# Kernel tuning notes

Measured on AMD Instinct MI355X. Metric: run time of the kernel, lower is better.

The kernel has to match this reference:

```python
import jax, jax.numpy as jnp
import numpy as np
from jax import lax

B, C_IN, H, W = 32, 3, 224, 224
EMBED = 768 // 4  # dim // 4 = 192
K = 3             # kernel_size
STRIDE = 2        # patch_stride
PAD = 1           # patch_padding
BN_EPS = 1e-5


def setup_inputs() -> dict:
    key = jax.random.key(0)
    kx, kw, kb, kg, kbeta = jax.random.split(key, 5)
    x = jax.random.normal(kx, (B, C_IN, H, W), dtype=jnp.float32)
    fan_in = C_IN * K * K
    bound = 1.0 / np.sqrt(fan_in)
    conv_w = jax.random.uniform(kw, (EMBED, C_IN, K, K), jnp.float32, -bound, bound)
    conv_b = jax.random.uniform(kb, (EMBED,), jnp.float32, -bound, bound)
    gamma = jnp.ones((EMBED,), jnp.float32)
    beta = jnp.zeros((EMBED,), jnp.float32)
    return {"x": x, "conv_w": conv_w, "conv_b": conv_b, "gamma": gamma, "beta": beta}


def _patch_embed(x, conv_w, conv_b, gamma, beta):
    # Conv2d(in_chans, embed_dim, k=3, stride=2, pad=1)
    y = lax.conv_general_dilated(
        x, conv_w,
        window_strides=(STRIDE, STRIDE),
        padding=[(PAD, PAD), (PAD, PAD)],
        dimension_numbers=("NCHW", "OIHW", "NCHW"),
    ) + conv_b[None, :, None, None]  # [B, EMBED, 112, 112]
    # BatchNorm2d (training mode: batch statistics, biased variance)
    mean = jnp.mean(y, axis=(0, 2, 3), keepdims=True)
    var = jnp.mean(jnp.square(y - mean), axis=(0, 2, 3), keepdims=True)
    y = (y - mean) * lax.rsqrt(var + BN_EPS)
    y = y * gamma[None, :, None, None] + beta[None, :, None, None]
    # GELU (torch default: exact erf form)
    y = jax.nn.gelu(y, approximate=False)
    # MaxPool2d(kernel=3, stride=2, padding=1)
    y = lax.reduce_window(
        y, -jnp.inf, lax.max,
        window_dimensions=(1, 1, 3, 3),
        window_strides=(1, 1, STRIDE, STRIDE),
        padding=[(0, 0), (0, 0), (PAD, PAD), (PAD, PAD)],
    )  # [B, EMBED, 56, 56]
    return y


def reference(x, conv_w, conv_b, gamma, beta):
    return _patch_embed(x, conv_w, conv_b, gamma, beta)
```

## Files before the change

### kernel.cpp

```cpp
#include <hip/hip_runtime.h>
#include <hip/hip_bf16.h>
#include <math.h>

#define B_   32
#define CIN  3
#define H_   224
#define W_   224
#define OC   192
#define OH   112
#define OW   112
#define PH   56
#define PW   56
#define NSP  (B_*OH*OW)
#define PLANE (OH*OW)

static __device__ __forceinline__ unsigned short f2bf(float f) {
    __hip_bfloat16 h = __float2bfloat16(f);
    return *reinterpret_cast<unsigned short*>(&h);
}
static __device__ __forceinline__ float bfbits2f(unsigned short u) {
    unsigned int v = ((unsigned int)u) << 16;
    return *reinterpret_cast<float*>(&v);
}
static __device__ __forceinline__ float bf_lo(unsigned int u) {
    unsigned int v = u << 16;
    return *reinterpret_cast<float*>(&v);
}
static __device__ __forceinline__ float bf_hi(unsigned int u) {
    unsigned int v = u & 0xffff0000u;
    return *reinterpret_cast<float*>(&v);
}

static __device__ __forceinline__ float fexp2(float x) {
#if __has_builtin(__builtin_amdgcn_exp2f)
    return __builtin_amdgcn_exp2f(x);
#else
    return exp2f(x);
#endif
}
static __device__ __forceinline__ float frcp(float x) {
#if __has_builtin(__builtin_amdgcn_rcpf)
    return __builtin_amdgcn_rcpf(x);
#else
    return 1.0f / x;
#endif
}

static __device__ __forceinline__ float fast_gelu(float x) {
    float x2 = x * x;
    float inner = fmaf(0.044715f * x2, x, x);
    float e = fexp2(inner * 2.3022082f);
    float r = frcp(1.0f + e);
    return x * (e * r);
}

__global__ void zero_stats(float* stats) {
    for (int i = threadIdx.x; i < 384; i += 256) stats[i] = 0.f;
}

__global__ __launch_bounds__(256) void conv_kernel(
    const float* __restrict__ x, const float* __restrict__ w,
    const float* __restrict__ bias, __hip_bfloat16* __restrict__ y)
{
    int g = blockIdx.x * 256 + threadIdx.x;
    int ow = g % OW;
    int t  = g / OW;
    int oh = t % OH;
    int b  = t / OH;

    int ih0 = 2 * oh - 1;
    int iw0 = 2 * ow - 1;

    float xv[CIN][3][3];
    #pragma unroll
    for (int c = 0; c < CIN; ++c) {
        #pragma unroll
        for (int r = 0; r < 3; ++r) {
            int ih = ih0 + r;
            bool rv = (ih >= 0) && (ih < H_);
            const float* xrow = x + (((size_t)b * CIN + c) * H_ + (rv ? ih : 0)) * W_;
            #pragma unroll
            for (int j = 0; j < 3; ++j) {
                int iw = iw0 + j;
                bool v = rv && (iw >= 0) && (iw < W_);
                xv[c][r][j] = v ? xrow[iw] : 0.f;
            }
        }
    }

    unsigned short* yp = reinterpret_cast<unsigned short*>(y) +
                         (size_t)b * OC * PLANE + oh * OW + ow;

    #pragma unroll 2
    for (int oc = 0; oc < OC; ++oc) {
        float a = bias[oc];
        const float* wp = w + oc * 27;
        #pragma unroll
        for (int c = 0; c < CIN; ++c)
            #pragma unroll
            for (int r = 0; r < 3; ++r)
                #pragma unroll
                for (int j = 0; j < 3; ++j)
                    a = fmaf(wp[c * 9 + r * 3 + j], xv[c][r][j], a);
        yp[(size_t)oc * PLANE] = f2bf(a);
    }
}

__global__ __launch_bounds__(256) void stats_kernel(
    const __hip_bfloat16* __restrict__ y, float* __restrict__ stats)
{
    int plane = blockIdx.x;
    int oc = plane % OC;
    const unsigned int* p =
        reinterpret_cast<const unsigned int*>(y) + plane * (PLANE / 2);

    float s = 0.f, s2 = 0.f;
    for (int ch = threadIdx.x; ch < PLANE / 8; ch += 256) {
        uint4 v = reinterpret_cast<const uint4*>(p)[ch];
        unsigned int u[4] = {v.x, v.y, v.z, v.w};
        #pragma unroll
        for (int k = 0; k < 4; ++k) {
            float lo = bf_lo(u[k]);
            float hi = bf_hi(u[k]);
            s  += lo + hi;
            s2 += lo * lo + hi * hi;
        }
    }

    __shared__ float ls[256], ls2[256];
    int tid = threadIdx.x;
    ls[tid] = s; ls2[tid] = s2;
    __syncthreads();
    for (int off = 128; off > 0; off >>= 1) {
        if (tid < off) { ls[tid] += ls[tid + off]; ls2[tid] += ls2[tid + off]; }
        __syncthreads();
    }
    if (tid == 0) {
        atomicAdd(&stats[oc], ls[0]);
        atomicAdd(&stats[OC + oc], ls2[0]);
    }
}

__global__ __launch_bounds__(256) void pool_kernel(
    const __hip_bfloat16* __restrict__ y, const float* __restrict__ stats,
    const float* __restrict__ gamma, const float* __restrict__ beta,
    float* __restrict__ out)
{
    int g = blockIdx.x * 256 + threadIdx.x;
    int j  = g % (PW / 4);
    int t  = g / (PW / 4);
    int ph = t % PH;
    int plane = t / PH;
    int oc = plane % OC;

    const unsigned int* p32 =
        reinterpret_cast<const unsigned int*>(y) + (size_t)plane * (PLANE / 2);

    int bi  = 4 * j - 1;
    int bi0 = (bi < 0) ? 0 : bi;

    float cmax[10], cmin[10];
    #pragma unroll
    for (int c = 0; c < 10; ++c) { cmax[c] = -INFINITY; cmin[c] = INFINITY; }

    #pragma unroll
    for (int rr = 0; rr < 3; ++rr) {
        int ih = 2 * ph - 1 + rr;
        if (ih >= 0) {
            const unsigned int* rp = p32 + ih * (OW / 2);
            unsigned int u0 = rp[bi0];
            unsigned int u1 = rp[bi + 1];
            unsigned int u2 = rp[bi + 2];
            unsigned int u3 = rp[bi + 3];
            unsigned int u4 = rp[bi + 4];
            float f0 = bf_lo(u0), f1 = bf_hi(u0);
            float f2 = bf_lo(u1), f3 = bf_hi(u1);
            float f4 = bf_lo(u2), f5 = bf_hi(u2);
            float f6 = bf_lo(u3), f7 = bf_hi(u3);
            float f8 = bf_lo(u4), f9 = bf_hi(u4);
            cmax[0] = fmaxf(cmax[0], f0); cmin[0] = fminf(cmin[0], f0);
            cmax[1] = fmaxf(cmax[1], f1); cmin[1] = fminf(cmin[1], f1);
            cmax[2] = fmaxf(cmax[2], f2); cmin[2] = fminf(cmin[2], f2);
            cmax[3] = fmaxf(cmax[3], f3); cmin[3] = fminf(cmin[3], f3);
            cmax[4] = fmaxf(cmax[4], f4); cmin[4] = fminf(cmin[4], f4);
            cmax[5] = fmaxf(cmax[5], f5); cmin[5] = fminf(cmin[5], f5);
            cmax[6] = fmaxf(cmax[6], f6); cmin[6] = fminf(cmin[6], f6);
            cmax[7] = fmaxf(cmax[7], f7); cmin[7] = fminf(cmin[7], f7);
            cmax[8] = fmaxf(cmax[8], f8); cmin[8] = fminf(cmin[8], f8);
            cmax[9] = fmaxf(cmax[9], f9); cmin[9] = fminf(cmin[9], f9);
        }
    }
    if (j == 0) { cmax[1] = -INFINITY; cmin[1] = INFINITY; }

    float mean = stats[oc] * (1.0f / (float)NSP);
    float var  = fmaf(-mean, mean, stats[OC + oc] * (1.0f / (float)NSP));
    float inv  = rsqrtf(var + 1e-5f);
    float sc   = gamma[oc] * inv;
    float sh   = fmaf(-mean, sc, beta[oc]);

    float4 res;
    float* rp4 = reinterpret_cast<float*>(&res);
    #pragma unroll
    for (int m = 0; m < 4; ++m) {
        float wmax = fmaxf(fmaxf(cmax[2 * m + 1], cmax[2 * m + 2]), cmax[2 * m + 3]);
        float wmin = fminf(fminf(cmin[2 * m + 1], cmin[2 * m + 2]), cmin[2 * m + 3]);
        float lo = fmaf(wmin, sc, sh);
        float hi = fmaf(wmax, sc, sh);
        rp4[m] = fmaxf(fast_gelu(lo), fast_gelu(hi));
    }

    *reinterpret_cast<float4*>(out + (size_t)plane * (PH * PW) + ph * PW + 4 * j) = res;
}

extern "C" void kernel_launch(void* const* d_in, const int* in_sizes, int n_in,
                              void* d_out, int out_size, void* d_ws, size_t ws_size,
                              hipStream_t stream) {
    const float* x     = (const float*)d_in[0];
    const float* w     = (const float*)d_in[1];
    const float* bias  = (const float*)d_in[2];
    const float* gamma = (const float*)d_in[3];
    const float* beta  = (const float*)d_in[4];
    float* out = (float*)d_out;

    float* stats = (float*)d_ws;
    __hip_bfloat16* y = (__hip_bfloat16*)((char*)d_ws + 4096);

    hipLaunchKernelGGL(zero_stats, dim3(1), dim3(256), 0, stream, stats);
    hipLaunchKernelGGL(conv_kernel, dim3(B_ * OH * OW / 256), dim3(256), 0, stream,
                       x, w, bias, y);
    hipLaunchKernelGGL(stats_kernel, dim3(B_ * OC), dim3(256), 0, stream, y, stats);
    hipLaunchKernelGGL(pool_kernel, dim3(B_ * OC * PH * (PW / 4) / 256), dim3(256), 0,
                       stream, y, stats, gamma, beta, out);
}
```

Baseline: 268.6 us.

## Register-block conv over 4 columns and tile maxpool into 2x8 outputs per thread

The conv kernel now has each thread compute 4 adjacent output columns for a 48-channel slice. It loads input rows with float4 reads and reuses the overlapping taps, so weights are read once per four outputs instead of once per output. The pool kernel now computes a 2x8 output tile per thread from 5 input rows loaded as uint4, which shares the overlapping window row between the two pooled output rows. The trade-off is that consecutive threads now map to different (batch, row) positions, which makes the conv loads and the bf16 stores strided rather than coalesced. It also uses more registers per thread.

```diff
diff --git a/kernel.cpp b/kernel.cpp
--- a/kernel.cpp
+++ b/kernel.cpp
@@ -18,10 +18,6 @@
     __hip_bfloat16 h = __float2bfloat16(f);
     return *reinterpret_cast<unsigned short*>(&h);
 }
-static __device__ __forceinline__ float bfbits2f(unsigned short u) {
-    unsigned int v = ((unsigned int)u) << 16;
-    return *reinterpret_cast<float*>(&v);
-}
 static __device__ __forceinline__ float bf_lo(unsigned int u) {
     unsigned int v = u << 16;
     return *reinterpret_cast<float*>(&v);
@@ -62,47 +58,83 @@
     const float* __restrict__ x, const float* __restrict__ w,
     const float* __restrict__ bias, __hip_bfloat16* __restrict__ y)
 {
-    int g = blockIdx.x * 256 + threadIdx.x;
-    int ow = g % OW;
-    int t  = g / OW;
-    int oh = t % OH;
-    int b  = t / OH;
+    int bx  = blockIdx.x;
+    int ocg = bx & 3;
+    int rem = bx >> 2;
+    int owg = rem % 28;
+    int sb  = rem / 28;
+    int pos = sb * 256 + threadIdx.x;
+    int oh  = pos % OH;
+    int b   = pos / OH;
 
     int ih0 = 2 * oh - 1;
-    int iw0 = 2 * ow - 1;
-
-    float xv[CIN][3][3];
-    #pragma unroll
-    for (int c = 0; c < CIN; ++c) {
-        #pragma unroll
-        for (int r = 0; r < 3; ++r) {
-            int ih = ih0 + r;
-            bool rv = (ih >= 0) && (ih < H_);
-            const float* xrow = x + (((size_t)b * CIN + c) * H_ + (rv ? ih : 0)) * W_;
-            #pragma unroll
-            for (int j = 0; j < 3; ++j) {
-                int iw = iw0 + j;
-                bool v = rv && (iw >= 0) && (iw < W_);
-                xv[c][r][j] = v ? xrow[iw] : 0.f;
-            }
-        }
-    }
-
+
+    float taps[CIN][3][9];
+    if (owg > 0) {
+        int s = 8 * owg - 4;
+        #pragma unroll
+        for (int c = 0; c < CIN; ++c) {
+            #pragma unroll
+            for (int r = 0; r < 3; ++r) {
+                int ih = ih0 + r;
+                bool rv = (ih >= 0) && (ih < H_);
+                const float* base =
+                    x + (((size_t)b * CIN + c) * H_ + (rv ? ih : 0)) * W_ + s;
+                float4 L0 = *reinterpret_cast<const float4*>(base);
+                float4 L1 = *reinterpret_cast<const float4*>(base + 4);
+                float4 L2 = *reinterpret_cast<const float4*>(base + 8);
+                float L[12] = {L0.x, L0.y, L0.z, L0.w, L1.x, L1.y, L1.z, L1.w,
+                               L2.x, L2.y, L2.z, L2.w};
+                #pragma unroll
+                for (int j = 0; j < 9; ++j)
+                    taps[c][r][j] = rv ? L[3 + j] : 0.f;
+            }
+        }
+    } else {
+        #pragma unroll
+        for (int c = 0; c < CIN; ++c) {
+            #pragma unroll
+            for (int r = 0; r < 3; ++r) {
+                int ih = ih0 + r;
+                bool rv = (ih >= 0) && (ih < H_);
+                const float* base =
+                    x + (((size_t)b * CIN + c) * H_ + (rv ? ih : 0)) * W_;
+                float4 L0 = *reinterpret_cast<const float4*>(base);
+                float4 L1 = *reinterpret_cast<const float4*>(base + 4);
+                float L[8] = {L0.x, L0.y, L0.z, L0.w, L1.x, L1.y, L1.z, L1.w};
+                taps[c][r][0] = 0.f;
+                #pragma unroll
+                for (int j = 1; j < 9; ++j)
+                    taps[c][r][j] = rv ? L[j - 1] : 0.f;
+            }
+        }
+    }
+
+    int oc0 = ocg * 48;
     unsigned short* yp = reinterpret_cast<unsigned short*>(y) +
-                         (size_t)b * OC * PLANE + oh * OW + ow;
+                         ((size_t)b * OC + oc0) * PLANE + oh * OW + 4 * owg;
 
     #pragma unroll 2
-    for (int oc = 0; oc < OC; ++oc) {
-        float a = bias[oc];
+    for (int l = 0; l < 48; ++l) {
+        int oc = oc0 + l;
+        float bs = bias[oc];
+        float a0 = bs, a1 = bs, a2 = bs, a3 = bs;
         const float* wp = w + oc * 27;
         #pragma unroll
         for (int c = 0; c < CIN; ++c)
             #pragma unroll
             for (int r = 0; r < 3; ++r)
                 #pragma unroll
-                for (int j = 0; j < 3; ++j)
-                    a = fmaf(wp[c * 9 + r * 3 + j], xv[c][r][j], a);
-        yp[(size_t)oc * PLANE] = f2bf(a);
+                for (int k = 0; k < 3; ++k) {
+                    float wv = wp[c * 9 + r * 3 + k];
+                    a0 = fmaf(wv, taps[c][r][k + 0], a0);
+                    a1 = fmaf(wv, taps[c][r][k + 2], a1);
+                    a2 = fmaf(wv, taps[c][r][k + 4], a2);
+                    a3 = fmaf(wv, taps[c][r][k + 6], a3);
+                }
+        ushort4 p;
+        p.x = f2bf(a0); p.y = f2bf(a1); p.z = f2bf(a2); p.w = f2bf(a3);
+        *reinterpret_cast<ushort4*>(yp + (size_t)l * PLANE) = p;
     }
 }
 
@@ -147,50 +179,60 @@
     float* __restrict__ out)
 {
     int g = blockIdx.x * 256 + threadIdx.x;
-    int j  = g % (PW / 4);
-    int t  = g / (PW / 4);
-    int ph = t % PH;
-    int plane = t / PH;
+    int j = g % 7;
+    int t = g / 7;
+    int i = t % 28;
+    int plane = t / 28;
     int oc = plane % OC;
 
-    const unsigned int* p32 =
-        reinterpret_cast<const unsigned int*>(y) + (size_t)plane * (PLANE / 2);
-
-    int bi  = 4 * j - 1;
-    int bi0 = (bi < 0) ? 0 : bi;
-
-    float cmax[10], cmin[10];
+    const unsigned short* py =
+        reinterpret_cast<const unsigned short*>(y) + (size_t)plane * PLANE;
+
+    float owmin[2][8], owmax[2][8];
     #pragma unroll
-    for (int c = 0; c < 10; ++c) { cmax[c] = -INFINITY; cmin[c] = INFINITY; }
+    for (int kk = 0; kk < 2; ++kk)
+        #pragma unroll
+        for (int m = 0; m < 8; ++m) { owmin[kk][m] = INFINITY; owmax[kk][m] = -INFINITY; }
 
     #pragma unroll
-    for (int rr = 0; rr < 3; ++rr) {
-        int ih = 2 * ph - 1 + rr;
+    for (int r = 0; r < 5; ++r) {
+        int ih = 4 * i - 1 + r;
         if (ih >= 0) {
-            const unsigned int* rp = p32 + ih * (OW / 2);
-            unsigned int u0 = rp[bi0];
-            unsigned int u1 = rp[bi + 1];
-            unsigned int u2 = rp[bi + 2];
-            unsigned int u3 = rp[bi + 3];
-            unsigned int u4 = rp[bi + 4];
-            float f0 = bf_lo(u0), f1 = bf_hi(u0);
-            float f2 = bf_lo(u1), f3 = bf_hi(u1);
-            float f4 = bf_lo(u2), f5 = bf_hi(u2);
-            float f6 = bf_lo(u3), f7 = bf_hi(u3);
-            float f8 = bf_lo(u4), f9 = bf_hi(u4);
-            cmax[0] = fmaxf(cmax[0], f0); cmin[0] = fminf(cmin[0], f0);
-            cmax[1] = fmaxf(cmax[1], f1); cmin[1] = fminf(cmin[1], f1);
-            cmax[2] = fmaxf(cmax[2], f2); cmin[2] = fminf(cmin[2], f2);
-            cmax[3] = fmaxf(cmax[3], f3); cmin[3] = fminf(cmin[3], f3);
-            cmax[4] = fmaxf(cmax[4], f4); cmin[4] = fminf(cmin[4], f4);
-            cmax[5] = fmaxf(cmax[5], f5); cmin[5] = fminf(cmin[5], f5);
-            cmax[6] = fmaxf(cmax[6], f6); cmin[6] = fminf(cmin[6], f6);
-            cmax[7] = fmaxf(cmax[7], f7); cmin[7] = fminf(cmin[7], f7);
-            cmax[8] = fmaxf(cmax[8], f8); cmin[8] = fminf(cmin[8], f8);
-            cmax[9] = fmaxf(cmax[9], f9); cmin[9] = fminf(cmin[9], f9);
-        }
-    }
-    if (j == 0) { cmax[1] = -INFINITY; cmin[1] = INFINITY; }
+            const uint4* rp = reinterpret_cast<const uint4*>(py + ih * OW + 16 * j - 8);
+            uint4 u0 = rp[0], u1 = rp[1], u2 = rp[2];
+            float L[24];
+            L[0]=bf_lo(u0.x); L[1]=bf_hi(u0.x); L[2]=bf_lo(u0.y); L[3]=bf_hi(u0.y);
+            L[4]=bf_lo(u0.z); L[5]=bf_hi(u0.z); L[6]=bf_lo(u0.w); L[7]=bf_hi(u0.w);
+            L[8]=bf_lo(u1.x); L[9]=bf_hi(u1.x); L[10]=bf_lo(u1.y); L[11]=bf_hi(u1.y);
+            L[12]=bf_lo(u1.z); L[13]=bf_hi(u1.z); L[14]=bf_lo(u1.w); L[15]=bf_hi(u1.w);
+            L[16]=bf_lo(u2.x); L[17]=bf_hi(u2.x); L[18]=bf_lo(u2.y); L[19]=bf_hi(u2.y);
+            L[20]=bf_lo(u2.z); L[21]=bf_hi(u2.z); L[22]=bf_lo(u2.w); L[23]=bf_hi(u2.w);
+
+            float l7min = (j == 0) ? INFINITY  : L[7];
+            float l7max = (j == 0) ? -INFINITY : L[7];
+
+            float hwmin[8], hwmax[8];
+            hwmin[0] = fminf(fminf(l7min, L[8]), L[9]);
+            hwmax[0] = fmaxf(fmaxf(l7max, L[8]), L[9]);
+            #pragma unroll
+            for (int m = 1; m < 8; ++m) {
+                hwmin[m] = fminf(fminf(L[7 + 2*m], L[8 + 2*m]), L[9 + 2*m]);
+                hwmax[m] = fmaxf(fmaxf(L[7 + 2*m], L[8 + 2*m]), L[9 + 2*m]);
+            }
+
+            #pragma unroll
+            for (int m = 0; m < 8; ++m) {
+                if (r <= 2) {
+                    owmin[0][m] = fminf(owmin[0][m], hwmin[m]);
+                    owmax[0][m] = fmaxf(owmax[0][m], hwmax[m]);
+                }
+                if (r >= 2) {
+                    owmin[1][m] = fminf(owmin[1][m], hwmin[m]);
+                    owmax[1][m] = fmaxf(owmax[1][m], hwmax[m]);
+                }
+            }
+        }
+    }
 
     float mean = stats[oc] * (1.0f / (float)NSP);
     float var  = fmaf(-mean, mean, stats[OC + oc] * (1.0f / (float)NSP));
@@ -198,18 +240,21 @@
     float sc   = gamma[oc] * inv;
     float sh   = fmaf(-mean, sc, beta[oc]);
 
-    float4 res;
-    float* rp4 = reinterpret_cast<float*>(&res);
+    float* ob = out + (size_t)plane * (PH * PW) + (2 * i) * PW + 8 * j;
     #pragma unroll
-    for (int m = 0; m < 4; ++m) {
-        float wmax = fmaxf(fmaxf(cmax[2 * m + 1], cmax[2 * m + 2]), cmax[2 * m + 3]);
-        float wmin = fminf(fminf(cmin[2 * m + 1], cmin[2 * m + 2]), cmin[2 * m + 3]);
-        float lo = fmaf(wmin, sc, sh);
-        float hi = fmaf(wmax, sc, sh);
-        rp4[m] = fmaxf(fast_gelu(lo), fast_gelu(hi));
-    }
-
-    *reinterpret_cast<float4*>(out + (size_t)plane * (PH * PW) + ph * PW + 4 * j) = res;
+    for (int kk = 0; kk < 2; ++kk) {
+        float res[8];
+        #pragma unroll
+        for (int m = 0; m < 8; ++m) {
+            float lo = fmaf(owmin[kk][m], sc, sh);
+            float hi = fmaf(owmax[kk][m], sc, sh);
+            res[m] = fmaxf(fast_gelu(lo), fast_gelu(hi));
+        }
+        float4 r0 = {res[0], res[1], res[2], res[3]};
+        float4 r1 = {res[4], res[5], res[6], res[7]};
+        *reinterpret_cast<float4*>(ob + kk * PW)     = r0;
+        *reinterpret_cast<float4*>(ob + kk * PW + 4) = r1;
+    }
 }
 
 extern "C" void kernel_launch(void* const* d_in, const int* in_sizes, int n_in,
@@ -226,9 +271,9 @@
     __hip_bfloat16* y = (__hip_bfloat16*)((char*)d_ws + 4096);
 
     hipLaunchKernelGGL(zero_stats, dim3(1), dim3(256), 0, stream, stats);
-    hipLaunchKernelGGL(conv_kernel, dim3(B_ * OH * OW / 256), dim3(256), 0, stream,
+    hipLaunchKernelGGL(conv_kernel, dim3(4 * 28 * 14), dim3(256), 0, stream,
                        x, w, bias, y);
     hipLaunchKernelGGL(stats_kernel, dim3(B_ * OC), dim3(256), 0, stream, y, stats);
-    hipLaunchKernelGGL(pool_kernel, dim3(B_ * OC * PH * (PW / 4) / 256), dim3(256), 0,
+    hipLaunchKernelGGL(pool_kernel, dim3(B_ * OC * PH * PW / 16 / 256), dim3(256), 0,
                        stream, y, stats, gamma, beta, out);
 }
```

Measured after the change: 534.2 us. +98.8%, slower.
